# Kernel tuning notes

Measured on AMD Instinct MI355X. Metric: run time of the kernel, lower is better.

## Reference

```python
import jax, jax.numpy as jnp
import numpy as np

B, S, E, H = 4, 2048, 1024, 16
D = E // H  # head_dim = 64

def setup_inputs() -> dict:
    key = jax.random.key(0)
    k1, k2, k3, k4, k5 = jax.random.split(key, 5)
    x = jax.random.normal(k1, (B, S, E), dtype=jnp.float32)
    # causal mask, broadcast over batch and heads; mask==0 -> -inf
    mask = jnp.tril(jnp.ones((S, S), dtype=jnp.int32))[None, None, :, :]
    Wqkv = jax.random.normal(k2, (E, 3 * E), dtype=jnp.float32) * (1.0 / np.sqrt(E))
    bqkv = jax.random.normal(k3, (3 * E,), dtype=jnp.float32) * 0.02
    Wo = jax.random.normal(k4, (E, E), dtype=jnp.float32) * (1.0 / np.sqrt(E))
    bo = jax.random.normal(k5, (E,), dtype=jnp.float32) * 0.02
    return {"x": x, "mask": mask, "Wqkv": Wqkv, "bqkv": bqkv, "Wo": Wo, "bo": bo}

def reference(x, mask, Wqkv, bqkv, Wo, bo):
    b, s, e = x.shape
    scale = 1.0 / np.sqrt(D)
    qkv = x @ Wqkv + bqkv                      # [b,s,3e]
    qkv = qkv.reshape(b, s, H, 3 * D).transpose(0, 2, 1, 3)  # [b,h,s,3d]
    q, k, v = jnp.split(qkv, 3, axis=-1)       # each [b,h,s,d]
    scores = jnp.einsum('bnqd,bnkd->bnqk', q, k) * scale
    scores = jnp.where(mask == 0, -jnp.inf, scores)
    probs = jax.nn.softmax(scores, axis=-1)
    attn = jnp.einsum('bnqk,bnkd->bnqd', probs, v)  # [b,h,s,d]
    # Faithful to source: reshape (b,h,s,d) -> (b,s,e) WITHOUT transposing back
    attn = attn.reshape(b, s, e)
    return attn @ Wo + bo
```

## Files before the change

### kernel.cpp

```cpp
#include <hip/hip_runtime.h>

typedef __attribute__((ext_vector_type(8))) short bf16x8;
typedef __attribute__((ext_vector_type(4))) float f32x4;
typedef __attribute__((ext_vector_type(2))) unsigned int u32x2;
typedef __attribute__((ext_vector_type(4))) unsigned int u32x4;

#define MFMA16(a, b, c) __builtin_amdgcn_mfma_f32_16x16x32_bf16((a), (b), (c), 0, 0, 0)

#define S_LEN 2048
#define NHEAD 16
#define DHEAD 64
#define BH    64
#define MROWS 8192

__device__ __forceinline__ unsigned short f2bf(float f) {
  unsigned int u = __builtin_bit_cast(unsigned int, f);
  u += 0x7FFFu + ((u >> 16) & 1u);
  return (unsigned short)(u >> 16);
}

__device__ __forceinline__ void gl_lds16(const void* g, void* l) {
  __builtin_amdgcn_global_load_lds(
      (const __attribute__((address_space(1))) void*)g,
      (__attribute__((address_space(3))) void*)l, 16, 0, 0);
}

__device__ __forceinline__ unsigned int pkbf(float lo, float hi) {
  unsigned int ulo = __builtin_bit_cast(unsigned int, lo) + 0x8000u;
  unsigned int uhi = __builtin_bit_cast(unsigned int, hi) + 0x8000u;
  return __builtin_amdgcn_perm(uhi, ulo, 0x07060302u);
}

__global__ __launch_bounds__(256) void cast_bf16(const float* __restrict__ src,
                                                 unsigned short* __restrict__ dst, int n) {
  int i = (blockIdx.x * 256 + threadIdx.x) * 4;
  if (i + 3 < n) {
    f32x4 v = *(const f32x4*)(src + i);
    unsigned long long pk =
        (unsigned long long)f2bf(v[0]) |
        ((unsigned long long)f2bf(v[1]) << 16) |
        ((unsigned long long)f2bf(v[2]) << 32) |
        ((unsigned long long)f2bf(v[3]) << 48);
    *(unsigned long long*)(dst + i) = pk;
  }
}

__global__ __launch_bounds__(256) void transpose_cast(const float* __restrict__ src,
                                                      unsigned short* __restrict__ dst,
                                                      int R, int C) {
  __shared__ float tile[32][33];
  int c0 = blockIdx.x * 32, r0 = blockIdx.y * 32;
  int tx = threadIdx.x, ty = threadIdx.y;
  for (int i = 0; i < 32; i += 8)
    tile[ty + i][tx] = src[(size_t)(r0 + ty + i) * C + c0 + tx];
  __syncthreads();
  for (int i = 0; i < 32; i += 8)
    dst[(size_t)(c0 + ty + i) * R + r0 + tx] = f2bf(tile[tx][ty + i]);
}

__global__ __launch_bounds__(256) void transpose_cast_qkv(const float* __restrict__ src,
                                                          unsigned short* __restrict__ dst) {
  __shared__ float tile[32][33];
  int c0 = blockIdx.x * 32, r0 = blockIdx.y * 32;
  int tx = threadIdx.x, ty = threadIdx.y;
  for (int i = 0; i < 32; i += 8)
    tile[ty + i][tx] = src[(size_t)(r0 + ty + i) * 3072 + c0 + tx];
  __syncthreads();
  for (int i = 0; i < 32; i += 8) {
    int oc = c0 + ty + i;
    int h = oc / 192, rr = oc % 192;
    int nc = ((rr >> 6) << 10) + (h << 6) + (rr & 63);
    dst[(size_t)nc * 1024 + r0 + tx] = f2bf(tile[tx][ty + i]);
  }
}

#define GEMM_CORE(A_, Bt_)                                                              \
  __shared__ unsigned short As[128 * 32];                                               \
  __shared__ unsigned short Bs[128 * 32];                                               \
  const int tid = threadIdx.x;                                                          \
  const int w = tid >> 6, lane = tid & 63, l15 = lane & 15, quad = lane >> 4;           \
  const int wm = w >> 1, wn = w & 1;                                                    \
  const int col0 = blockIdx.x * 128, row0 = blockIdx.y * 128;                           \
  f32x4 acc[4][4] = {};                                                                 \
  for (int kt = 0; kt < 32; ++kt) {                                                     \
    const int k0 = kt * 32;                                                             \
    for (int p = 0; p < 2; ++p) {                                                       \
      int c = p * 256 + tid;                                                            \
      int m = c >> 2, k8 = (c & 3) * 8;                                                 \
      void* ldsA = (char*)As + (size_t)(p * 256 + (tid & 192)) * 16;                    \
      void* ldsB = (char*)Bs + (size_t)(p * 256 + (tid & 192)) * 16;                    \
      gl_lds16(A_ + (size_t)(row0 + m) * 1024 + k0 + k8, ldsA);                         \
      gl_lds16(Bt_ + (size_t)(col0 + m) * 1024 + k0 + k8, ldsB);                        \
    }                                                                                   \
    __syncthreads();                                                                    \
    bf16x8 af[4], bfr[4];                                                               \
    for (int i = 0; i < 4; ++i)                                                         \
      af[i] = *(const bf16x8*)&As[(wm * 64 + i * 16 + l15) * 32 + quad * 8];            \
    for (int j = 0; j < 4; ++j)                                                         \
      bfr[j] = *(const bf16x8*)&Bs[(wn * 64 + j * 16 + l15) * 32 + quad * 8];           \
    for (int i = 0; i < 4; ++i)                                                         \
      for (int j = 0; j < 4; ++j)                                                       \
        acc[i][j] = MFMA16(af[i], bfr[j], acc[i][j]);                                   \
    __syncthreads();                                                                    \
  }

__global__ __launch_bounds__(256) void gemm_qkv(const unsigned short* __restrict__ A,
                                                const unsigned short* __restrict__ Bt,
                                                const float* __restrict__ bias,
                                                unsigned short* __restrict__ Qb,
                                                unsigned short* __restrict__ Kb,
                                                unsigned short* __restrict__ Vtb) {
  __shared__ float Es[4][16][66];
  GEMM_CORE(A, Bt)
  const int bx = col0 >> 7;
  float bv[4];
  #pragma unroll
  for (int j = 0; j < 4; ++j) {
    int nc = col0 + wn * 64 + j * 16 + l15;
    int oc = ((nc >> 6) & 15) * 192 + (nc >> 10) * 64 + (nc & 63);
    bv[j] = bias[oc];
  }
  const float sc = (bx < 8) ? 0.18033688011112042f : 1.0f;
  const int b = row0 >> 11;
  const int srow0 = (row0 & 2047) + wm * 64;
  const int h = ((col0 + wn * 64) >> 6) & 15;
  float (*Ew)[66] = Es[w];

  if (bx < 16) {
    const int lr = lane >> 2, ch2 = lane & 3, d0 = ch2 * 16;
    unsigned short* base = (bx < 8 ? Qb : Kb) + ((size_t)(b * 16 + h) * 2048) * 64;
    for (int i = 0; i < 4; ++i) {
      #pragma unroll
      for (int j = 0; j < 4; ++j)
        #pragma unroll
        for (int r = 0; r < 4; ++r)
          Ew[quad * 4 + r][j * 16 + l15] = (acc[i][j][r] + bv[j]) * sc;
      float v[16];
      #pragma unroll
      for (int c = 0; c < 4; ++c)
        *(f32x4*)&v[4 * c] = *(const f32x4*)&Ew[lr][d0 + 4 * c];
      u32x4 pk0 = {pkbf(v[0], v[1]), pkbf(v[2], v[3]), pkbf(v[4], v[5]), pkbf(v[6], v[7])};
      u32x4 pk1 = {pkbf(v[8], v[9]), pkbf(v[10], v[11]), pkbf(v[12], v[13]), pkbf(v[14], v[15])};
      unsigned short* dst = base + (size_t)(srow0 + i * 16 + lr) * 64 + d0;
      *(u32x4*)dst = pk0;
      *(u32x4*)(dst + 8) = pk1;
    }
  } else {
    const int d = lane;
    unsigned short* base = Vtb + ((size_t)(b * 16 + h) * 64 + d) * 2048;
    for (int i = 0; i < 4; ++i) {
      #pragma unroll
      for (int j = 0; j < 4; ++j)
        #pragma unroll
        for (int r = 0; r < 4; ++r)
          Ew[quad * 4 + r][j * 16 + l15] = acc[i][j][r] + bv[j];
      float e[16];
      #pragma unroll
      for (int k = 0; k < 16; ++k) e[k] = Ew[k][d];
      u32x4 pk0 = {pkbf(e[0], e[1]), pkbf(e[2], e[3]), pkbf(e[4], e[5]), pkbf(e[6], e[7])};
      u32x4 pk1 = {pkbf(e[8], e[9]), pkbf(e[10], e[11]), pkbf(e[12], e[13]), pkbf(e[14], e[15])};
      unsigned short* dst = base + srow0 + i * 16;
      *(u32x4*)dst = pk0;
      *(u32x4*)(dst + 8) = pk1;
    }
  }
}

__global__ __launch_bounds__(256) void gemm_out(const unsigned short* __restrict__ A,
                                                const unsigned short* __restrict__ Bt,
                                                const float* __restrict__ bias,
                                                float* __restrict__ out) {
  GEMM_CORE(A, Bt)
  for (int i = 0; i < 4; ++i) {
    int grow = row0 + wm * 64 + i * 16 + quad * 4;
    for (int j = 0; j < 4; ++j) {
      int gcol = col0 + wn * 64 + j * 16 + l15;
      float bvv = bias[gcol];
      for (int r = 0; r < 4; ++r)
        out[(size_t)(grow + r) * 1024 + gcol] = acc[i][j][r] + bvv;
    }
  }
}

__global__ __launch_bounds__(256) void attn_kernel(const unsigned short* __restrict__ Qb,
                                                   const unsigned short* __restrict__ Kb,
                                                   const unsigned short* __restrict__ Vtb,
                                                   unsigned short* __restrict__ attnout) {
  __shared__ unsigned short K0[64 * 32], K1[64 * 32];
  __shared__ unsigned short V0[64 * 32], V1[64 * 32];
  __shared__ unsigned short P0[4][4][512], P1[4][4][512];
  __shared__ float Lbc[4][64];

  const int tid = threadIdx.x;
  const int w = tid >> 6, lane = tid & 63, l15 = lane & 15, quad = lane >> 4;
  const int i2 = blockIdx.x >> 6;
  const int jj = ((i2 & 1) << 1) | ((i2 >> 1) & 1);
  const int qt = (i2 & 4) ? jj : 7 - jj;
  const int bh = blockIdx.x & 63;
  const int q0w = qt * 256 + w * 64;

  const unsigned short* Qg = Qb + (size_t)bh * S_LEN * DHEAD;
  const unsigned short* Kg = Kb + (size_t)bh * S_LEN * DHEAD;
  const unsigned short* Vg = Vtb + (size_t)bh * DHEAD * S_LEN;

  bf16x8 qf[4][2];
  #pragma unroll
  for (int sub = 0; sub < 4; ++sub) {
    const unsigned short* p = Qg + (size_t)(q0w + sub * 16 + l15) * DHEAD + quad * 8;
    qf[sub][0] = *(const bf16x8*)p;
    qf[sub][1] = *(const bf16x8*)(p + 32);
  }

  const int srow = tid >> 2, sc8 = (tid & 3) * 8;
  const unsigned short* kgb = Kg + srow * 64 + sc8;
  const unsigned short* vgb = Vg + (size_t)srow * S_LEN + sc8;
  const int wKo = srow * 32 + sc8;

  const int psw = (l15 & 3) ^ ((l15 >> 2) & 3);
  const int pw0 = l15 * 32 + (((quad >> 1) ^ psw) << 3) + ((quad & 1) << 2);
  const int pw1 = l15 * 32 + ((((quad >> 1) + 2) ^ psw) << 3) + ((quad & 1) << 2);
  const int pro = l15 * 32 + ((quad ^ psw) << 3);
  const int kvo = l15 * 32 + quad * 8;

  f32x4 oacc[4][4] = {};
  float lacc[4] = {0.f, 0.f, 0.f, 0.f};

  const int ktdiag = 4 * qt;
  const int nkt = ktdiag + 4;

  bf16x8 kr0 = *(const bf16x8*)kgb, kr1 = *(const bf16x8*)(kgb + 32);
  bf16x8 vr0 = *(const bf16x8*)vgb, vr1 = *(const bf16x8*)(vgb + 32);

  for (int kt = 0; kt < nkt; ++kt) {
    *(bf16x8*)&K0[wKo] = kr0;  *(bf16x8*)&K1[wKo] = kr1;
    *(bf16x8*)&V0[wKo] = vr0;  *(bf16x8*)&V1[wKo] = vr1;
    __syncthreads();
    if (kt + 1 < nkt) {
      const unsigned short* kp = kgb + (kt + 1) * 4096;
      const unsigned short* vp = vgb + (kt + 1) * 64;
      kr0 = *(const bf16x8*)kp;  kr1 = *(const bf16x8*)(kp + 32);
      vr0 = *(const bf16x8*)vp;  vr1 = *(const bf16x8*)(vp + 32);
    }

    const int t = kt - ktdiag;
    const bool act = (t < 0) || (w >= t);

    if (act) {
      if (t < 0) {
        #pragma unroll
        for (int jk = 0; jk < 4; ++jk) {
          bf16x8 kf0 = *(const bf16x8*)&K0[jk * 512 + kvo];
          bf16x8 kf1 = *(const bf16x8*)&K1[jk * 512 + kvo];
          #pragma unroll
          for (int sub = 0; sub < 4; ++sub) {
            f32x4 z = {};
            z = MFMA16(kf0, qf[sub][0], z);
            z = MFMA16(kf1, qf[sub][1], z);
            float e0 = __builtin_amdgcn_exp2f(z[0]);
            float e1 = __builtin_amdgcn_exp2f(z[1]);
            float e2 = __builtin_amdgcn_exp2f(z[2]);
            float e3 = __builtin_amdgcn_exp2f(z[3]);
            lacc[sub] += (e0 + e1) + (e2 + e3);
            unsigned short* pd = (jk < 2) ? P0[w][sub] : P1[w][sub];
            *(u32x2*)&pd[(jk & 1) ? pw1 : pw0] = (u32x2){pkbf(e0, e1), pkbf(e2, e3)};
          }
        }
      } else {
        const bool dg = (t == w);
        #pragma unroll
        for (int jk = 0; jk < 4; ++jk) {
          bf16x8 kf0 = *(const bf16x8*)&K0[jk * 512 + kvo];
          bf16x8 kf1 = *(const bf16x8*)&K1[jk * 512 + kvo];
          #pragma unroll
          for (int sub = 0; sub < 4; ++sub) {
            unsigned short* pd = (jk < 2) ? P0[w][sub] : P1[w][sub];
            unsigned int* dst = (unsigned int*)&pd[(jk & 1) ? pw1 : pw0];
            if (dg && jk > sub) { *(u32x2*)dst = (u32x2){0u, 0u}; continue; }
            f32x4 z = {};
            z = MFMA16(kf0, qf[sub][0], z);
            z = MFMA16(kf1, qf[sub][1], z);
            if (dg && jk == sub) {
              #pragma unroll
              for (int r = 0; r < 4; ++r)
                if (quad * 4 + r > l15) z[r] = -3e38f;
            }
            float e0 = __builtin_amdgcn_exp2f(z[0]);
            float e1 = __builtin_amdgcn_exp2f(z[1]);
            float e2 = __builtin_amdgcn_exp2f(z[2]);
            float e3 = __builtin_amdgcn_exp2f(z[3]);
            lacc[sub] += (e0 + e1) + (e2 + e3);
            *(u32x2*)dst = (u32x2){pkbf(e0, e1), pkbf(e2, e3)};
          }
        }
      }

      bf16x8 pf[4][2];
      #pragma unroll
      for (int sub = 0; sub < 4; ++sub) {
        pf[sub][0] = *(const bf16x8*)&P0[w][sub][pro];
        pf[sub][1] = *(const bf16x8*)&P1[w][sub][pro];
      }
      #pragma unroll
      for (int dt = 0; dt < 4; ++dt) {
        bf16x8 vb0 = *(const bf16x8*)&V0[dt * 512 + kvo];
        bf16x8 vb1 = *(const bf16x8*)&V1[dt * 512 + kvo];
        #pragma unroll
        for (int sub = 0; sub < 4; ++sub) {
          oacc[sub][dt] = MFMA16(pf[sub][0], vb0, oacc[sub][dt]);
          oacc[sub][dt] = MFMA16(pf[sub][1], vb1, oacc[sub][dt]);
        }
      }
    }
    __syncthreads();
  }

  #pragma unroll
  for (int sub = 0; sub < 4; ++sub) {
    float l = lacc[sub];
    l += __shfl_xor(l, 16);
    l += __shfl_xor(l, 32);
    if (quad == 0) Lbc[w][sub * 16 + l15] = l;
  }
  #pragma unroll
  for (int sub = 0; sub < 4; ++sub) {
    f32x4 l4 = *(const f32x4*)&Lbc[w][sub * 16 + quad * 4];
    int qbase = q0w + sub * 16 + quad * 4;
    unsigned short* dst = attnout + ((size_t)bh * S_LEN + qbase) * DHEAD;
    #pragma unroll
    for (int r = 0; r < 4; ++r) {
      float inv = __builtin_amdgcn_rcpf(l4[r]);
      #pragma unroll
      for (int dt = 0; dt < 4; ++dt)
        dst[(size_t)r * DHEAD + dt * 16 + l15] = f2bf(oacc[sub][dt][r] * inv);
    }
  }
}

extern "C" void kernel_launch(void* const* d_in, const int* in_sizes, int n_in,
                              void* d_out, int out_size, void* d_ws, size_t ws_size,
                              hipStream_t stream) {
  const float* x    = (const float*)d_in[0];
  const float* Wqkv = (const float*)d_in[2];
  const float* bqkv = (const float*)d_in[3];
  const float* Wo   = (const float*)d_in[4];
  const float* bo   = (const float*)d_in[5];
  float* out = (float*)d_out;

  char* ws = (char*)d_ws;
  unsigned short* Xbf   = (unsigned short*)(ws);
  unsigned short* WqkvT = (unsigned short*)(ws + 16777216);
  unsigned short* WoT   = (unsigned short*)(ws + 23068672);
  unsigned short* Qb    = (unsigned short*)(ws + 25165824);
  unsigned short* Kb    = (unsigned short*)(ws + 41943040);
  unsigned short* Vtb   = (unsigned short*)(ws + 58720256);
  unsigned short* Attn  = (unsigned short*)(ws + 75497472);

  cast_bf16<<<8192, 256, 0, stream>>>(x, Xbf, MROWS * 1024);
  transpose_cast_qkv<<<dim3(96, 32), dim3(32, 8), 0, stream>>>(Wqkv, WqkvT);
  transpose_cast<<<dim3(32, 32), dim3(32, 8), 0, stream>>>(Wo, WoT, 1024, 1024);
  gemm_qkv<<<dim3(24, 64), 256, 0, stream>>>(Xbf, WqkvT, bqkv, Qb, Kb, Vtb);
  attn_kernel<<<512, 256, 0, stream>>>(Qb, Kb, Vtb, Attn);
  gemm_out<<<dim3(8, 64), 256, 0, stream>>>(Attn, WoT, bo, out);
}
```

Measured before the change: 266.4 us.

## Rewrite QKV GEMM with 256x256 tiles, double-buffered async LDS staging and swizzle

```diff
diff --git a/kernel.cpp b/kernel.cpp
--- a/kernel.cpp
+++ b/kernel.cpp
@@ -104,15 +104,148 @@
     __syncthreads();                                                                    \
   }
 
-__global__ __launch_bounds__(256) void gemm_qkv(const unsigned short* __restrict__ A,
-                                                const unsigned short* __restrict__ Bt,
-                                                const float* __restrict__ bias,
-                                                unsigned short* __restrict__ Qb,
-                                                unsigned short* __restrict__ Kb,
-                                                unsigned short* __restrict__ Vtb) {
-  __shared__ float Es[4][16][66];
-  GEMM_CORE(A, Bt)
-  const int bx = col0 >> 7;
+
+#define VM4 asm volatile("s_waitcnt vmcnt(4)" ::: "memory")
+#define VM0 asm volatile("s_waitcnt vmcnt(0)" ::: "memory")
+#define LGKM0 asm volatile("s_waitcnt lgkmcnt(0)" ::: "memory")
+#define BAR __builtin_amdgcn_s_barrier()
+#define SB  __builtin_amdgcn_sched_barrier(0)
+
+#define STAGE_AH(T, H)                                                           \
+  do {                                                                           \
+    char* lb_ = SHB + (((T) & 1) * 65536 + (H) * 16384) + stgo;                  \
+    const unsigned short* gs_ = a_src + (size_t)(H) * 131072 + (T) * 64;         \
+    gl_lds16(gs_, lb_);                                                          \
+    gl_lds16(gs_ + 65536, lb_ + 8192);                                           \
+  } while (0)
+#define STAGE_BH(T, H)                                                           \
+  do {                                                                           \
+    char* lb_ = SHB + (((T) & 1) * 65536 + 32768 + (H) * 16384) + stgo;          \
+    const unsigned short* gs_ = b_src + (size_t)(H) * 131072 + (T) * 64;         \
+    gl_lds16(gs_, lb_);                                                          \
+    gl_lds16(gs_ + 65536, lb_ + 8192);                                           \
+  } while (0)
+
+#define RD_A4(BUF, MH, KH)                                                       \
+  do {                                                                           \
+    const char* p_ = SHB + (BUF) * 65536 + awave + (MH) * 8192 + (ck ^ ((KH) * 64)); \
+    af0 = *(const bf16x8*)(p_);                                                  \
+    af1 = *(const bf16x8*)(p_ + 2048);                                           \
+    af2 = *(const bf16x8*)(p_ + 4096);                                           \
+    af3 = *(const bf16x8*)(p_ + 6144);                                           \
+  } while (0)
+#define RD_B4(BUF, S, KH)                                                        \
+  do {                                                                           \
+    const char* p_ = SHB + (BUF) * 65536 + bwave + (ck ^ ((KH) * 64));           \
+    bq##S##0 = *(const bf16x8*)(p_);                                             \
+    bq##S##1 = *(const bf16x8*)(p_ + 2048);                                      \
+    bq##S##2 = *(const bf16x8*)(p_ + 4096);                                      \
+    bq##S##3 = *(const bf16x8*)(p_ + 6144);                                      \
+  } while (0)
+
+#define MF16(MH, S)                                                              \
+  __builtin_amdgcn_s_setprio(1);                                                 \
+  acc[(MH)*4+0][0] = MFMA16(af0, bq##S##0, acc[(MH)*4+0][0]);                    \
+  acc[(MH)*4+0][1] = MFMA16(af0, bq##S##1, acc[(MH)*4+0][1]);                    \
+  acc[(MH)*4+0][2] = MFMA16(af0, bq##S##2, acc[(MH)*4+0][2]);                    \
+  acc[(MH)*4+0][3] = MFMA16(af0, bq##S##3, acc[(MH)*4+0][3]);                    \
+  acc[(MH)*4+1][0] = MFMA16(af1, bq##S##0, acc[(MH)*4+1][0]);                    \
+  acc[(MH)*4+1][1] = MFMA16(af1, bq##S##1, acc[(MH)*4+1][1]);                    \
+  acc[(MH)*4+1][2] = MFMA16(af1, bq##S##2, acc[(MH)*4+1][2]);                    \
+  acc[(MH)*4+1][3] = MFMA16(af1, bq##S##3, acc[(MH)*4+1][3]);                    \
+  acc[(MH)*4+2][0] = MFMA16(af2, bq##S##0, acc[(MH)*4+2][0]);                    \
+  acc[(MH)*4+2][1] = MFMA16(af2, bq##S##1, acc[(MH)*4+2][1]);                    \
+  acc[(MH)*4+2][2] = MFMA16(af2, bq##S##2, acc[(MH)*4+2][2]);                    \
+  acc[(MH)*4+2][3] = MFMA16(af2, bq##S##3, acc[(MH)*4+2][3]);                    \
+  acc[(MH)*4+3][0] = MFMA16(af3, bq##S##0, acc[(MH)*4+3][0]);                    \
+  acc[(MH)*4+3][1] = MFMA16(af3, bq##S##1, acc[(MH)*4+3][1]);                    \
+  acc[(MH)*4+3][2] = MFMA16(af3, bq##S##2, acc[(MH)*4+3][2]);                    \
+  acc[(MH)*4+3][3] = MFMA16(af3, bq##S##3, acc[(MH)*4+3][3]);                    \
+  __builtin_amdgcn_s_setprio(0)
+
+#define KTILE4(BUF, T, GA, GB, WAIT_)                                            \
+  {                                                            \
+    RD_A4(BUF, 0, 0);                                                            \
+    RD_B4(BUF, A, 0);                                                            \
+    if (GA) STAGE_AH((T) + 1, 0);                                                \
+    SB; BAR;                                                                     \
+    LGKM0; SB;                                                                   \
+    MF16(0, A);                                                                  \
+    SB; BAR;                                                                     \
+  }                                                                              \
+  {                                                            \
+    RD_A4(BUF, 0, 1);                                                            \
+    RD_B4(BUF, B, 1);                                                            \
+    if (GA) STAGE_AH((T) + 1, 1);                                                \
+    SB; BAR;                                                                     \
+    LGKM0; SB;                                                                   \
+    MF16(0, B);                                                                  \
+    SB; BAR;                                                                     \
+  }                                                                              \
+  {                                                            \
+    RD_A4(BUF, 1, 0);                                                            \
+    if (GB) STAGE_BH((T) + 2, 0);                                                \
+    SB; BAR;                                                                     \
+    LGKM0; SB;                                                                   \
+    MF16(1, A);                                                                  \
+    SB; BAR;                                                                     \
+  }                                                                              \
+  {                                                            \
+    RD_A4(BUF, 1, 1);                                                            \
+    if (GB) STAGE_BH((T) + 2, 1);                                                \
+    SB; BAR;                                                                     \
+    LGKM0; SB;                                                                   \
+    MF16(1, B);                                                                  \
+    WAIT_;                                                                       \
+    SB; BAR;                                                                     \
+  }
+
+__global__ __launch_bounds__(512, 2) void gemm_qkv(const unsigned short* __restrict__ A,
+                                                   const unsigned short* __restrict__ Bt,
+                                                   const float* __restrict__ bias,
+                                                   unsigned short* __restrict__ Qb,
+                                                   unsigned short* __restrict__ Kb,
+                                                   unsigned short* __restrict__ Vtb) {
+  __shared__ unsigned short SH[65536];
+  char* SHB = (char*)SH;
+  const int tid = threadIdx.x;
+  const int w = tid >> 6, lane = tid & 63, l15 = lane & 15, quad = lane >> 4;
+  const int wm = w >> 2, wn = w & 3;
+  const int g = ((blockIdx.x & 7) * 48) + (blockIdx.x >> 3);
+  const int bx = g % 12, by = g / 12;
+  const int col0 = bx << 8, row0 = by << 8;
+
+  const int ck = (quad ^ (l15 & 7)) << 4;
+  const int awave = wm * 16384 + l15 * 128;
+  const int bwave = 32768 + (wn >> 1) * 16384 + (wn & 1) * 8192 + l15 * 128;
+
+  const int stgc = (tid & 7) ^ ((tid >> 3) & 7);
+  const unsigned short* a_src = A + (size_t)(row0 + (tid >> 3)) * 1024 + stgc * 8;
+  const unsigned short* b_src = Bt + (size_t)(col0 + (tid >> 3)) * 1024 + stgc * 8;
+  const int stgo = (tid & ~63) * 16;
+
+  f32x4 acc[8][4] = {};
+  bf16x8 af0, af1, af2, af3;
+  bf16x8 bqA0, bqA1, bqA2, bqA3, bqB0, bqB1, bqB2, bqB3;
+
+  STAGE_AH(0, 0); STAGE_AH(0, 1); STAGE_BH(0, 0); STAGE_BH(0, 1);
+  STAGE_BH(1, 0); STAGE_BH(1, 1);
+  VM4; SB; BAR; SB;
+
+  #pragma unroll 1
+  for (int jj = 0; jj < 7; ++jj) {
+    const int T0 = 2 * jj;
+    KTILE4(0, T0,     1, 1, VM4)
+    KTILE4(1, T0 + 1, 1, 1, VM4)
+  }
+  KTILE4(0, 14, 1, 0, VM0)
+  KTILE4(1, 15, 0, 0, (void)0)
+  __syncthreads();
+
+  const int which = col0 >> 10;
+  const int h = ((col0 + wn * 64) >> 6) & 15;
+  const int b = row0 >> 11;
+  const int srow0 = (row0 & 2047) + wm * 128;
   float bv[4];
   #pragma unroll
   for (int j = 0; j < 4; ++j) {
@@ -120,46 +253,45 @@
     int oc = ((nc >> 6) & 15) * 192 + (nc >> 10) * 64 + (nc & 63);
     bv[j] = bias[oc];
   }
-  const float sc = (bx < 8) ? 0.18033688011112042f : 1.0f;
-  const int b = row0 >> 11;
-  const int srow0 = (row0 & 2047) + wm * 64;
-  const int h = ((col0 + wn * 64) >> 6) & 15;
-  float (*Ew)[66] = Es[w];
-
-  if (bx < 16) {
-    const int lr = lane >> 2, ch2 = lane & 3, d0 = ch2 * 16;
-    unsigned short* base = (bx < 8 ? Qb : Kb) + ((size_t)(b * 16 + h) * 2048) * 64;
-    for (int i = 0; i < 4; ++i) {
+  float* Ew = (float*)SHB + w * 1072;
+
+  if (which < 2) {
+    const float sc = (which == 0) ? 0.18033688011112042f : 1.0f;
+    const int lr = lane >> 2, d0 = (lane & 3) * 16;
+    unsigned short* base = (which == 0 ? Qb : Kb) + ((size_t)(b * 16 + h) * 2048 + srow0) * 64;
+    #pragma unroll
+    for (int i = 0; i < 8; ++i) {
       #pragma unroll
       for (int j = 0; j < 4; ++j)
         #pragma unroll
         for (int r = 0; r < 4; ++r)
-          Ew[quad * 4 + r][j * 16 + l15] = (acc[i][j][r] + bv[j]) * sc;
+          Ew[(quad * 4 + r) * 66 + j * 16 + l15] = (acc[i][j][r] + bv[j]) * sc;
       float v[16];
       #pragma unroll
       for (int c = 0; c < 4; ++c)
-        *(f32x4*)&v[4 * c] = *(const f32x4*)&Ew[lr][d0 + 4 * c];
+        *(f32x4*)&v[4 * c] = *(const f32x4*)&Ew[lr * 66 + d0 + 4 * c];
       u32x4 pk0 = {pkbf(v[0], v[1]), pkbf(v[2], v[3]), pkbf(v[4], v[5]), pkbf(v[6], v[7])};
       u32x4 pk1 = {pkbf(v[8], v[9]), pkbf(v[10], v[11]), pkbf(v[12], v[13]), pkbf(v[14], v[15])};
-      unsigned short* dst = base + (size_t)(srow0 + i * 16 + lr) * 64 + d0;
+      unsigned short* dst = base + (size_t)(i * 16 + lr) * 64 + d0;
       *(u32x4*)dst = pk0;
       *(u32x4*)(dst + 8) = pk1;
     }
   } else {
     const int d = lane;
-    unsigned short* base = Vtb + ((size_t)(b * 16 + h) * 64 + d) * 2048;
-    for (int i = 0; i < 4; ++i) {
+    unsigned short* base = Vtb + ((size_t)(b * 16 + h) * 64 + d) * 2048 + srow0;
+    #pragma unroll
+    for (int i = 0; i < 8; ++i) {
       #pragma unroll
       for (int j = 0; j < 4; ++j)
         #pragma unroll
         for (int r = 0; r < 4; ++r)
-          Ew[quad * 4 + r][j * 16 + l15] = acc[i][j][r] + bv[j];
+          Ew[(quad * 4 + r) * 66 + j * 16 + l15] = acc[i][j][r] + bv[j];
       float e[16];
       #pragma unroll
-      for (int k = 0; k < 16; ++k) e[k] = Ew[k][d];
+      for (int k = 0; k < 16; ++k) e[k] = Ew[k * 66 + d];
       u32x4 pk0 = {pkbf(e[0], e[1]), pkbf(e[2], e[3]), pkbf(e[4], e[5]), pkbf(e[6], e[7])};
       u32x4 pk1 = {pkbf(e[8], e[9]), pkbf(e[10], e[11]), pkbf(e[12], e[13]), pkbf(e[14], e[15])};
-      unsigned short* dst = base + srow0 + i * 16;
+      unsigned short* dst = base + i * 16;
       *(u32x4*)dst = pk0;
       *(u32x4*)(dst + 8) = pk1;
     }
@@ -358,7 +490,7 @@
   cast_bf16<<<8192, 256, 0, stream>>>(x, Xbf, MROWS * 1024);
   transpose_cast_qkv<<<dim3(96, 32), dim3(32, 8), 0, stream>>>(Wqkv, WqkvT);
   transpose_cast<<<dim3(32, 32), dim3(32, 8), 0, stream>>>(Wo, WoT, 1024, 1024);
-  gemm_qkv<<<dim3(24, 64), 256, 0, stream>>>(Xbf, WqkvT, bqkv, Qb, Kb, Vtb);
+  gemm_qkv<<<384, 512, 0, stream>>>(Xbf, WqkvT, bqkv, Qb, Kb, Vtb);
   attn_kernel<<<512, 256, 0, stream>>>(Qb, Kb, Vtb, Attn);
   gemm_out<<<dim3(8, 64), 256, 0, stream>>>(Attn, WoT, bo, out);
 }
```

Result: no change. 269.8 us (+1.3%).
